# Kernel optimization log

Hardware: AMD Instinct MI355X
Metric: run time of the kernel (lower is better)

Reference implementation:

```python
import jax, jax.numpy as jnp
import numpy as np

B, S, D = 2, 2048, 2048
H, KV, HD = 32, 8, 64
REP = H // KV


def rotate_half(t):
    t1, t2 = t[..., : t.shape[-1] // 2], t[..., t.shape[-1] // 2 :]
    return jnp.concatenate((-t2, t1), axis=-1)


def setup_inputs() -> dict:
    key = jax.random.key(0)
    kx, kq, kk, kv, ko = jax.random.split(key, 5)
    x = jax.random.normal(kx, (B, S, D), dtype=jnp.float32) * 0.02
    # RoPE tables: shape [S, HD//2]; forward concatenates [cos, cos] to reach HD
    inv_freq = 1.0 / (10000.0 ** (np.arange(0, HD, 2, dtype=np.float32) / HD))
    freqs = np.outer(np.arange(S, dtype=np.float32), inv_freq)
    cos = jnp.asarray(np.cos(freqs), dtype=jnp.float32)
    sin = jnp.asarray(np.sin(freqs), dtype=jnp.float32)
    # causal additive mask [1,1,S,S]
    causal = np.tril(np.ones((S, S), dtype=bool))
    mask = jnp.asarray(np.where(causal, 0.0, -1e9).astype(np.float32))[None, None]
    s = 0.02
    wq = jax.random.normal(kq, (H * HD, D), dtype=jnp.float32) * s
    wk = jax.random.normal(kk, (KV * HD, D), dtype=jnp.float32) * s
    wv = jax.random.normal(kv, (KV * HD, D), dtype=jnp.float32) * s
    wo = jax.random.normal(ko, (D, H * HD), dtype=jnp.float32) * s
    return {"x": x, "cos": cos, "sin": sin, "mask": mask,
            "wq": wq, "wk": wk, "wv": wv, "wo": wo}


def reference(x, cos, sin, mask, wq, wk, wv, wo):
    b, s, d = x.shape
    # QKV projections (Linear with bias=False: x @ W^T)
    q = jnp.einsum("bsd,ed->bse", x, wq).reshape(b, s, H, HD)
    k = jnp.einsum("bsd,ed->bse", x, wk).reshape(b, s, KV, HD)
    v = jnp.einsum("bsd,ed->bse", x, wv).reshape(b, s, KV, HD)
    # RoPE: cos/sin [S, HD//2] -> [1, S, 1, HD]
    cc = jnp.concatenate([cos[:s], cos[:s]], axis=-1)[None, :, None, :]
    ss = jnp.concatenate([sin[:s], sin[:s]], axis=-1)[None, :, None, :]
    q = q * cc + rotate_half(q) * ss
    k = k * cc + rotate_half(k) * ss
    # GQA: group q heads by kv head (implicit broadcast instead of repeat_kv)
    q = q.transpose(0, 2, 1, 3).reshape(b, KV, REP, s, HD)  # [B,KV,REP,S,HD]
    k = k.transpose(0, 2, 1, 3)                              # [B,KV,S,HD]
    v = v.transpose(0, 2, 1, 3)                              # [B,KV,S,HD]
    scores = jnp.einsum("bkrqd,bksd->bkrqs", q, k) / np.sqrt(HD)
    scores = scores + mask[:, :, None, :, :]  # broadcast over rep dim
    probs = jax.nn.softmax(scores.astype(jnp.float32), axis=-1).astype(q.dtype)
    out = jnp.einsum("bkrqs,bksd->bkrqd", probs, v)
    out = out.transpose(0, 3, 1, 2, 4).reshape(b, s, H * HD)  # [B,S,H*HD]
    return jnp.einsum("bse,de->bsd", out, wo)
```

## Files before the change

### kernel.cpp

```cpp
#include <hip/hip_runtime.h>
#include <stdint.h>

#define DEV __device__ __forceinline__

typedef __bf16 bf16;
typedef __bf16 bf16x8 __attribute__((ext_vector_type(8)));
typedef __bf16 bf16x4v __attribute__((ext_vector_type(4)));
typedef float f32x4 __attribute__((ext_vector_type(4)));
typedef float f32x16 __attribute__((ext_vector_type(16)));
typedef int int2v __attribute__((ext_vector_type(2)));

constexpr int Bb = 2, Ss = 2048, Dd = 2048, Hh = 32, KVh = 8, HDd = 64;
constexpr int Mm = Bb * Ss;
constexpr int EQ = Hh * HDd;
constexpr int EKV = KVh * HDd;
constexpr int Ee = EQ + 2 * EKV;

DEV void gload16(const void* g, void* l) {
  __builtin_amdgcn_global_load_lds((const __attribute__((address_space(1))) uint32_t*)g,
                                   (__attribute__((address_space(3))) uint32_t*)l, 16, 0, 0);
}

#if __has_builtin(__builtin_amdgcn_exp2f)
DEV float exp2_fast(float x) { return __builtin_amdgcn_exp2f(x); }
#else
DEV float exp2_fast(float x) {
  float r;
  asm("v_exp_f32 %0, %1\n\ts_nop 0" : "=v"(r) : "v"(x));
  return r;
}
#endif
DEV uint32_t cvtpk(float lo, float hi) {
  uint32_t w;
  asm("v_cvt_pk_bf16_f32 %0, %1, %2" : "=v"(w) : "v"(lo), "v"(hi));
  return w;
}
DEV int2v pswap(uint32_t a, uint32_t b) {
  return __builtin_amdgcn_permlane32_swap((int)a, (int)b, false, false);
}
DEV float fu(uint32_t u) { union { uint32_t u; float f; } c; c.u = u; return c.f; }
DEV uint32_t uf(float f) { union { float f; uint32_t u; } c; c.f = f; return c.u; }

__global__ void cvt_kernel(const float* __restrict__ x, const float* __restrict__ wq,
                           const float* __restrict__ wk, const float* __restrict__ wv,
                           const float* __restrict__ wo,
                           bf16* __restrict__ xb, bf16* __restrict__ wqkvb,
                           bf16* __restrict__ wob) {
  const long NX = (long)Mm * Dd;
  const long NQ = (long)EQ * Dd;
  const long NK = (long)EKV * Dd;
  const long NO = (long)Dd * EQ;
  const long total4 = (NX + NQ + 2 * NK + NO) / 4;
  for (long i = (long)blockIdx.x * blockDim.x + threadIdx.x; i < total4;
       i += (long)gridDim.x * blockDim.x) {
    long e = i * 4;
    const float* src; bf16* dst;
    if (e < NX)                { src = x + e;                       dst = xb + e; }
    else if (e < NX + NQ)      { long o = e - NX;                   src = wq + o; dst = wqkvb + o; }
    else if (e < NX + NQ + NK) { long o = e - NX - NQ;              src = wk + o; dst = wqkvb + NQ + o; }
    else if (e < NX + NQ + 2*NK){ long o = e - NX - NQ - NK;        src = wv + o; dst = wqkvb + NQ + NK + o; }
    else                       { long o = e - NX - NQ - 2*NK;       src = wo + o; dst = wob + o; }
    float4 v = *(const float4*)src;
    bf16x4v b;
    b.x = (bf16)v.x; b.y = (bf16)v.y; b.z = (bf16)v.z; b.w = (bf16)v.w;
    *(bf16x4v*)dst = b;
  }
}

__global__ __launch_bounds__(512, 4)
void gemm1_kernel(const bf16* __restrict__ A, const bf16* __restrict__ Bt,
                  bf16* __restrict__ Cb, int Mn, int Nn, int Kn) {
  __shared__ __align__(16) bf16 As[2][128 * 64];
  __shared__ __align__(16) bf16 Bs[2][192 * 64];
  const int tid = threadIdx.x, wid = tid >> 6, lane = tid & 63;
  const int g = lane >> 4, c = lane & 15;
  const int wm = wid >> 2, wn = wid & 3;

  const int xcd = (int)blockIdx.x & 7;
  const int idx = (int)blockIdx.x >> 3;
  const int bi = (xcd >> 1) * 8 + (idx >> 3);
  const int bj = (xcd & 1) * 8 + (idx & 7);
  const long arow0 = (long)bi * 128, brow0 = (long)bj * 192;

  const int srow = tid >> 3, schk = tid & 7;
  const int cs = schk ^ (srow & 7);

  f32x4 acc[4][3] = {};

#pragma unroll
  for (int q = 0; q < 2; ++q)
    gload16(A + (arow0 + q * 64 + srow) * Kn + cs * 8,
            (char*)&As[0][0] + q * 8192 + tid * 16);
#pragma unroll
  for (int q = 0; q < 3; ++q)
    gload16(Bt + (brow0 + q * 64 + srow) * Kn + cs * 8,
            (char*)&Bs[0][0] + q * 8192 + tid * 16);
  __syncthreads();

  const int NT = Kn >> 6;
  for (int kt = 0; kt < NT; ++kt) {
    const char* pa = (const char*)&As[kt & 1][0];
    const char* pb = (const char*)&Bs[kt & 1][0];
    char* na = (char*)&As[(kt + 1) & 1][0];
    char* nb = (char*)&Bs[(kt + 1) & 1][0];
    const bool more = (kt + 1 < NT);

    bf16x8 af[4][2];
#pragma unroll
    for (int i2 = 0; i2 < 4; ++i2)
#pragma unroll
      for (int ks = 0; ks < 2; ++ks) {
        int r = wm * 64 + i2 * 16 + c;
        af[i2][ks] = *(const bf16x8*)(pa + r * 128 + (((ks * 4 + g) ^ (r & 7)) << 4));
      }
    bf16x8 bfr[2];
#pragma unroll
    for (int ks = 0; ks < 2; ++ks) {
      int r = 0 * 64 + wn * 16 + c;
      bfr[ks] = *(const bf16x8*)(pb + r * 128 + (((ks * 4 + g) ^ (r & 7)) << 4));
    }
    if (more) {
      gload16(A + (arow0 + 0 * 64 + srow) * Kn + (kt + 1) * 64 + cs * 8,
              na + 0 * 8192 + tid * 16);
      gload16(A + (arow0 + 1 * 64 + srow) * Kn + (kt + 1) * 64 + cs * 8,
              na + 1 * 8192 + tid * 16);
      gload16(Bt + (brow0 + 0 * 64 + srow) * Kn + (kt + 1) * 64 + cs * 8,
              nb + 0 * 8192 + tid * 16);
    }
    asm volatile("s_waitcnt lgkmcnt(0)" ::: "memory");
    __builtin_amdgcn_s_setprio(1);
#pragma unroll
    for (int i2 = 0; i2 < 4; ++i2)
#pragma unroll
      for (int ks = 0; ks < 2; ++ks)
        acc[i2][0] = __builtin_amdgcn_mfma_f32_16x16x32_bf16(af[i2][ks], bfr[ks],
                                                             acc[i2][0], 0, 0, 0);
    __builtin_amdgcn_s_setprio(0);
    if (more) asm volatile("s_waitcnt vmcnt(4)" ::: "memory");
    else      asm volatile("s_waitcnt vmcnt(1)" ::: "memory");
    __builtin_amdgcn_s_barrier();

#pragma unroll
    for (int ks = 0; ks < 2; ++ks) {
      int r = 1 * 64 + wn * 16 + c;
      bfr[ks] = *(const bf16x8*)(pb + r * 128 + (((ks * 4 + g) ^ (r & 7)) << 4));
    }
    if (more)
      gload16(Bt + (brow0 + 1 * 64 + srow) * Kn + (kt + 1) * 64 + cs * 8,
              nb + 1 * 8192 + tid * 16);
    asm volatile("s_waitcnt lgkmcnt(0)" ::: "memory");
    __builtin_amdgcn_s_setprio(1);
#pragma unroll
    for (int i2 = 0; i2 < 4; ++i2)
#pragma unroll
      for (int ks = 0; ks < 2; ++ks)
        acc[i2][1] = __builtin_amdgcn_mfma_f32_16x16x32_bf16(af[i2][ks], bfr[ks],
                                                             acc[i2][1], 0, 0, 0);
    __builtin_amdgcn_s_setprio(0);
    if (more) asm volatile("s_waitcnt vmcnt(4)" ::: "memory");
    else      asm volatile("s_waitcnt vmcnt(0)" ::: "memory");
    __builtin_amdgcn_s_barrier();

#pragma unroll
    for (int ks = 0; ks < 2; ++ks) {
      int r = 2 * 64 + wn * 16 + c;
      bfr[ks] = *(const bf16x8*)(pb + r * 128 + (((ks * 4 + g) ^ (r & 7)) << 4));
    }
    if (more)
      gload16(Bt + (brow0 + 2 * 64 + srow) * Kn + (kt + 1) * 64 + cs * 8,
              nb + 2 * 8192 + tid * 16);
    asm volatile("s_waitcnt lgkmcnt(0)" ::: "memory");
    __builtin_amdgcn_s_setprio(1);
#pragma unroll
    for (int i2 = 0; i2 < 4; ++i2)
#pragma unroll
      for (int ks = 0; ks < 2; ++ks)
        acc[i2][2] = __builtin_amdgcn_mfma_f32_16x16x32_bf16(af[i2][ks], bfr[ks],
                                                             acc[i2][2], 0, 0, 0);
    __builtin_amdgcn_s_setprio(0);
    if (more) {
      asm volatile("s_waitcnt vmcnt(2)" ::: "memory");
      __builtin_amdgcn_s_barrier();
    }
  }

#pragma unroll
  for (int i = 0; i < 4; ++i)
#pragma unroll
    for (int j = 0; j < 3; ++j)
#pragma unroll
      for (int r = 0; r < 4; ++r) {
        long row = arow0 + wm * 64 + i * 16 + 4 * g + r;
        long col = brow0 + j * 64 + wn * 16 + c;
        Cb[row * Nn + col] = (bf16)acc[i][j][r];
      }
}

__global__ __launch_bounds__(512, 4)
void gemm2_kernel(const bf16* __restrict__ A, const bf16* __restrict__ Bt,
                  float* __restrict__ Cf, int Mn, int Nn, int Kn) {
  __shared__ __align__(16) bf16 As[2][128 * 64];
  __shared__ __align__(16) bf16 Bs[2][128 * 64];
  const int tid = threadIdx.x, wid = tid >> 6, lane = tid & 63;
  const int g = lane >> 4, c = lane & 15;
  const int wm = wid >> 2, wn = wid & 3;

  const int xcd = (int)blockIdx.x & 7;
  const int idx = (int)blockIdx.x >> 3;
  const int bi = (xcd >> 1) * 8 + (idx >> 3);
  const int bj = (xcd & 1) * 8 + (idx & 7);
  const long arow0 = (long)bi * 128, brow0 = (long)bj * 128;

  const int srow = tid >> 3, schk = tid & 7;
  const int cs = schk ^ (srow & 7);

  f32x4 acc[4][2] = {};

#pragma unroll
  for (int q = 0; q < 2; ++q) {
    gload16(A + (arow0 + q * 64 + srow) * Kn + cs * 8,
            (char*)&As[0][0] + q * 8192 + tid * 16);
    gload16(Bt + (brow0 + q * 64 + srow) * Kn + cs * 8,
            (char*)&Bs[0][0] + q * 8192 + tid * 16);
  }
  __syncthreads();

  const int NT = Kn >> 6;
  for (int kt = 0; kt < NT; ++kt) {
    const char* pa = (const char*)&As[kt & 1][0];
    const char* pb = (const char*)&Bs[kt & 1][0];
    char* na = (char*)&As[(kt + 1) & 1][0];
    char* nb = (char*)&Bs[(kt + 1) & 1][0];
    const bool more = (kt + 1 < NT);

    bf16x8 af[4][2];
#pragma unroll
    for (int i2 = 0; i2 < 4; ++i2)
#pragma unroll
      for (int ks = 0; ks < 2; ++ks) {
        int r = wm * 64 + i2 * 16 + c;
        af[i2][ks] = *(const bf16x8*)(pa + r * 128 + (((ks * 4 + g) ^ (r & 7)) << 4));
      }
    bf16x8 bfr[2];
#pragma unroll
    for (int ks = 0; ks < 2; ++ks) {
      int r = 0 * 64 + wn * 16 + c;
      bfr[ks] = *(const bf16x8*)(pb + r * 128 + (((ks * 4 + g) ^ (r & 7)) << 4));
    }
    if (more) {
      gload16(A + (arow0 + 0 * 64 + srow) * Kn + (kt + 1) * 64 + cs * 8,
              na + 0 * 8192 + tid * 16);
      gload16(Bt + (brow0 + 0 * 64 + srow) * Kn + (kt + 1) * 64 + cs * 8,
              nb + 0 * 8192 + tid * 16);
    }
    asm volatile("s_waitcnt lgkmcnt(0)" ::: "memory");
    __builtin_amdgcn_s_setprio(1);
#pragma unroll
    for (int i2 = 0; i2 < 4; ++i2)
#pragma unroll
      for (int ks = 0; ks < 2; ++ks)
        acc[i2][0] = __builtin_amdgcn_mfma_f32_16x16x32_bf16(af[i2][ks], bfr[ks],
                                                             acc[i2][0], 0, 0, 0);
    __builtin_amdgcn_s_setprio(0);
    if (more) asm volatile("s_waitcnt vmcnt(2)" ::: "memory");
    else      asm volatile("s_waitcnt vmcnt(0)" ::: "memory");
    __builtin_amdgcn_s_barrier();

#pragma unroll
    for (int ks = 0; ks < 2; ++ks) {
      int r = 1 * 64 + wn * 16 + c;
      bfr[ks] = *(const bf16x8*)(pb + r * 128 + (((ks * 4 + g) ^ (r & 7)) << 4));
    }
    if (more) {
      gload16(A + (arow0 + 1 * 64 + srow) * Kn + (kt + 1) * 64 + cs * 8,
              na + 1 * 8192 + tid * 16);
      gload16(Bt + (brow0 + 1 * 64 + srow) * Kn + (kt + 1) * 64 + cs * 8,
              nb + 1 * 8192 + tid * 16);
    }
    asm volatile("s_waitcnt lgkmcnt(0)" ::: "memory");
    __builtin_amdgcn_s_setprio(1);
#pragma unroll
    for (int i2 = 0; i2 < 4; ++i2)
#pragma unroll
      for (int ks = 0; ks < 2; ++ks)
        acc[i2][1] = __builtin_amdgcn_mfma_f32_16x16x32_bf16(af[i2][ks], bfr[ks],
                                                             acc[i2][1], 0, 0, 0);
    __builtin_amdgcn_s_setprio(0);
    if (more) {
      asm volatile("s_waitcnt vmcnt(1)" ::: "memory");
      __builtin_amdgcn_s_barrier();
    }
  }

#pragma unroll
  for (int i = 0; i < 4; ++i)
#pragma unroll
    for (int j = 0; j < 2; ++j)
#pragma unroll
      for (int r = 0; r < 4; ++r) {
        long row = arow0 + wm * 64 + i * 16 + 4 * g + r;
        long col = brow0 + j * 64 + wn * 16 + c;
        Cf[row * Nn + col] = acc[i][j][r];
      }
}

__global__ void kv_prep_kernel(const bf16* __restrict__ qkv, const float* __restrict__ cosT,
                               const float* __restrict__ sinT, bf16* __restrict__ kout,
                               bf16* __restrict__ vtb) {
  if (blockIdx.x < 512) {
    __shared__ __align__(16) unsigned short tile[64][72];
    int blk = blockIdx.x;
    int st = blk & 31, kvh = (blk >> 5) & 7, b = blk >> 8;
    int s0 = st * 64;
    int t = threadIdx.x;
#pragma unroll
    for (int rep = 0; rep < 2; ++rep) {
      int idx = t + rep * 256;
      int r = idx >> 3, cb = idx & 7;
      const bf16* src = qkv + ((long)(b * Ss + s0 + r)) * Ee + EQ + EKV + kvh * 64 + cb * 8;
      *(uint4*)&tile[r][cb * 8] = *(const uint4*)src;
    }
    __syncthreads();
#pragma unroll
    for (int rep = 0; rep < 2; ++rep) {
      int idx = t + rep * 256;
      int dd = idx >> 3, scb = idx & 7;
      union { unsigned short u[8]; uint4 v; } pk;
#pragma unroll
      for (int j = 0; j < 8; ++j) pk.u[j] = tile[scb * 8 + j][dd];
      long dst = ((long)((b * KVh + kvh) * 64 + dd)) * Ss + s0 + scb * 8;
      *(uint4*)&vtb[dst] = pk.v;
    }
  } else {
    int tid = (int)(blockIdx.x - 512) * blockDim.x + threadIdx.x;
    int d = tid & 31;
    int h = (tid >> 5) & (KVh - 1);
    int m = tid >> 8;
    if (m >= Mm) return;
    int s = m & (Ss - 1), b = m >> 11;
    float lo = (float)qkv[(long)m * Ee + EQ + h * 64 + d];
    float hi = (float)qkv[(long)m * Ee + EQ + h * 64 + d + 32];
    float cs = cosT[s * 32 + d], sn = sinT[s * 32 + d];
    long base = (((long)(b * KVh + h)) * Ss + s) * 64;
    kout[base + d]      = (bf16)(lo * cs - hi * sn);
    kout[base + d + 32] = (bf16)(hi * cs + lo * sn);
  }
}

__global__ __launch_bounds__(512)
void attn_kernel(const bf16* __restrict__ qkv, const float* __restrict__ cosT,
                 const float* __restrict__ sinT, const bf16* __restrict__ k,
                 const bf16* __restrict__ vt, bf16* __restrict__ o) {
  __shared__ __align__(16) bf16 Kt[2][2][64 * 64];
  __shared__ __align__(16) bf16 Vt[2][2][64 * 64];
  constexpr float SCL = 0.18033688f;

  const int tid = threadIdx.x, qw = tid >> 6, lane = tid & 63;
  const int ql = lane & 31, hi = lane >> 5;
  const int g6 = (int)(blockIdx.x >> 6);
  const int qt = (g6 < 4) ? (7 - g6) : (g6 - 4);
  const int bh = blockIdx.x & 63;
  const int b = bh >> 5, h = bh & 31;
  const int kvh = h >> 2;
  const int q0 = qt * 256;
  const int qw_q0 = q0 + qw * 32;

  const bf16* kbase = k + ((long)(b * KVh + kvh)) * Ss * 64;
  const bf16* vbase = vt + ((long)(b * KVh + kvh)) * 64 * Ss;

  const int srow = tid >> 3, scb = tid & 7;
  const int scbs = scb ^ (srow & 7);
  const int sdst = tid * 16;

  bf16x8 qf[4];
  {
    const int s_row = q0 + qw * 32 + ql;
    const bf16* qrow = qkv + ((long)(b * Ss + s_row)) * Ee + h * 64 + 8 * hi;
    bf16x8 qraw[4];
#pragma unroll
    for (int ks = 0; ks < 4; ++ks) qraw[ks] = *(const bf16x8*)(qrow + 16 * ks);
    float cs8[2][8], sn8[2][8];
#pragma unroll
    for (int ks2 = 0; ks2 < 2; ++ks2) {
      const float* cp = cosT + s_row * 32 + 16 * ks2 + 8 * hi;
      const float* sp = sinT + s_row * 32 + 16 * ks2 + 8 * hi;
      *(float4*)&cs8[ks2][0] = *(const float4*)cp;
      *(float4*)&cs8[ks2][4] = *(const float4*)(cp + 4);
      *(float4*)&sn8[ks2][0] = *(const float4*)sp;
      *(float4*)&sn8[ks2][4] = *(const float4*)(sp + 4);
    }
#pragma unroll
    for (int ks2 = 0; ks2 < 2; ++ks2)
#pragma unroll
      for (int j = 0; j < 8; ++j) {
        float lo = (float)qraw[ks2][j], hv = (float)qraw[ks2 + 2][j];
        qf[ks2][j]     = (bf16)((lo * cs8[ks2][j] - hv * sn8[ks2][j]) * SCL);
        qf[ks2 + 2][j] = (bf16)((hv * cs8[ks2][j] + lo * sn8[ks2][j]) * SCL);
      }
  }

  bf16x8 bones;
#pragma unroll
  for (int j = 0; j < 8; ++j) bones[j] = (bf16)1.0f;

  gload16(kbase + (long)srow * 64 + scbs * 8, (char*)&Kt[0][0][0] + sdst);
  gload16(kbase + ((long)64 + srow) * 64 + scbs * 8, (char*)&Kt[0][1][0] + sdst);
  gload16(vbase + (long)srow * Ss + scbs * 8, (char*)&Vt[0][0][0] + sdst);
  gload16(vbase + (long)srow * Ss + 64 + scbs * 8, (char*)&Vt[0][1][0] + sdst);
  __syncthreads();

  f32x16 Oacc0 = {}, Oacc1 = {}, lacc = {};
  const int qa = qw_q0 + ql;
  const int nt = 4 * qt + 4;
  const int ntp = nt >> 1;
  const int tdiag = qw_q0 >> 6;

  int cur = 0;
  for (int pp = 0; pp < ntp; ++pp) {
    if (pp + 1 < ntp) {
      int nb = cur ^ 1;
      long t0 = (long)(2 * pp + 2) * 64;
      gload16(kbase + (t0 + srow) * 64 + scbs * 8, (char*)&Kt[nb][0][0] + sdst);
      gload16(kbase + (t0 + 64 + srow) * 64 + scbs * 8, (char*)&Kt[nb][1][0] + sdst);
      gload16(vbase + (long)srow * Ss + t0 + scbs * 8, (char*)&Vt[nb][0][0] + sdst);
      gload16(vbase + (long)srow * Ss + t0 + 64 + scbs * 8, (char*)&Vt[nb][1][0] + sdst);
    }

#pragma unroll
    for (int half = 0; half < 2; ++half) {
      const int t = 2 * pp + half;
      if (64 * t < qw_q0 + 32) {
        f32x16 s0 = {}, s1 = {};
        const char* kt = (const char*)&Kt[cur][half][0];
#pragma unroll
        for (int ks = 0; ks < 4; ++ks) {
          int chk = ((2 * ks + hi) ^ (ql & 7)) << 4;
          bf16x8 kf0 = *(const bf16x8*)(kt + ql * 128 + chk);
          bf16x8 kf1 = *(const bf16x8*)(kt + (32 + ql) * 128 + chk);
          s0 = __builtin_amdgcn_mfma_f32_32x32x16_bf16(kf0, qf[ks], s0, 0, 0, 0);
          s1 = __builtin_amdgcn_mfma_f32_32x32x16_bf16(kf1, qf[ks], s1, 0, 0, 0);
        }

        if (t == tdiag) {
#pragma unroll
          for (int r = 0; r < 16; ++r) {
            int kv0 = t * 64 + (r & 3) + 8 * (r >> 2) + 4 * hi;
            if (kv0 > qa)      s0[r] = -1e30f;
            if (kv0 + 32 > qa) s1[r] = -1e30f;
          }
        }

#pragma unroll
        for (int r = 0; r < 16; ++r) {
          s0[r] = exp2_fast(s0[r]);
          s1[r] = exp2_fast(s1[r]);
        }

        const char* vtb0 = (const char*)&Vt[cur][half][0];
#pragma unroll
        for (int ks = 0; ks < 4; ++ks) {
          uint32_t pk01, pk23, pk45, pk67;
          if (ks < 2) {
            const int rb = (ks & 1) * 8;
            pk01 = cvtpk(s0[rb + 0], s0[rb + 1]);
            pk23 = cvtpk(s0[rb + 2], s0[rb + 3]);
            pk45 = cvtpk(s0[rb + 4], s0[rb + 5]);
            pk67 = cvtpk(s0[rb + 6], s0[rb + 7]);
          } else {
            const int rb = (ks & 1) * 8;
            pk01 = cvtpk(s1[rb + 0], s1[rb + 1]);
            pk23 = cvtpk(s1[rb + 2], s1[rb + 3]);
            pk45 = cvtpk(s1[rb + 4], s1[rb + 5]);
            pk67 = cvtpk(s1[rb + 6], s1[rb + 7]);
          }
          int2v w02 = pswap(pk01, pk45);
          int2v w13 = pswap(pk23, pk67);
          union { uint32_t u[4]; bf16x8 v; } pa;
          pa.u[0] = (uint32_t)w02.x; pa.u[1] = (uint32_t)w13.x;
          pa.u[2] = (uint32_t)w02.y; pa.u[3] = (uint32_t)w13.y;

          int chk = ((2 * ks + hi) ^ (ql & 7)) << 4;
          bf16x8 vf0 = *(const bf16x8*)(vtb0 + ql * 128 + chk);
          bf16x8 vf1 = *(const bf16x8*)(vtb0 + (32 + ql) * 128 + chk);
          Oacc0 = __builtin_amdgcn_mfma_f32_32x32x16_bf16(pa.v, vf0, Oacc0, 0, 0, 0);
          Oacc1 = __builtin_amdgcn_mfma_f32_32x32x16_bf16(pa.v, vf1, Oacc1, 0, 0, 0);
          lacc  = __builtin_amdgcn_mfma_f32_32x32x16_bf16(pa.v, bones, lacc, 0, 0, 0);
        }
      }
    }

    __syncthreads();
    cur ^= 1;
  }

#pragma unroll
  for (int r = 0; r < 16; ++r) {
    int qrow = (r & 3) + 8 * (r >> 2) + 4 * hi;
    float li = 1.0f / lacc[r];
    long orow = (long)b * Ss + q0 + 32 * qw + qrow;
    o[orow * EQ + h * 64 + ql]      = (bf16)(Oacc0[r] * li);
    o[orow * EQ + h * 64 + 32 + ql] = (bf16)(Oacc1[r] * li);
  }
}

extern "C" void kernel_launch(void* const* d_in, const int* in_sizes, int n_in,
                              void* d_out, int out_size, void* d_ws, size_t ws_size,
                              hipStream_t stream) {
  const float* x    = (const float*)d_in[0];
  const float* cosT = (const float*)d_in[1];
  const float* sinT = (const float*)d_in[2];
  const float* wq   = (const float*)d_in[4];
  const float* wk   = (const float*)d_in[5];
  const float* wv   = (const float*)d_in[6];
  const float* wo   = (const float*)d_in[7];

  if (ws_size < 104857600u) return;

  char* ws = (char*)d_ws;
  bf16* xb    = (bf16*)(ws + 0);
  bf16* wqkvb = (bf16*)(ws + 16777216);
  bf16* wob   = (bf16*)(ws + 29360128);
  bf16* qkvb  = (bf16*)(ws + 37748736);
  bf16* kb    = (bf16*)(ws + 79691776);
  bf16* vtb   = (bf16*)(ws + 83886080);
  bf16* attnb = (bf16*)(ws + 88080384);
  float* outp = (float*)d_out;

  cvt_kernel<<<dim3(2048), dim3(256), 0, stream>>>(x, wq, wk, wv, wo, xb, wqkvb, wob);
  gemm1_kernel<<<dim3((Mm / 128) * (Ee / 192)), dim3(512), 0, stream>>>(
      xb, wqkvb, qkvb, Mm, Ee, Dd);
  kv_prep_kernel<<<dim3(512 + (Mm * KVh * 32) / 256), dim3(256), 0, stream>>>(
      qkvb, cosT, sinT, kb, vtb);
  attn_kernel<<<dim3(512), dim3(512), 0, stream>>>(qkvb, cosT, sinT, kb, vtb, attnb);
  gemm2_kernel<<<dim3((Mm / 128) * (EQ / 128)), dim3(512), 0, stream>>>(
      attnb, wob, outp, Mm, EQ, EQ);
}
```

Measured before the change: 158.6 us.

## Triple-buffer K tiles and prefetch two steps ahead with partial vmcnt waits

Adds a third LDS buffer for K so K tiles are prefetched two iterations ahead while V stays double-buffered. The full __syncthreads is replaced by an s_waitcnt vmcnt(2)/vmcnt(0) plus a raw s_barrier, so the loads for the furthest K tile can stay in flight across the barrier. This aims to hide global-to-LDS load latency behind the MFMA work. It raises LDS use, which may lower occupancy, and relies on the counts of outstanding loads being right.

```diff
diff --git a/kernel.cpp b/kernel.cpp
--- a/kernel.cpp
+++ b/kernel.cpp
@@ -351,7 +351,7 @@
 void attn_kernel(const bf16* __restrict__ qkv, const float* __restrict__ cosT,
                  const float* __restrict__ sinT, const bf16* __restrict__ k,
                  const bf16* __restrict__ vt, bf16* __restrict__ o) {
-  __shared__ __align__(16) bf16 Kt[2][2][64 * 64];
+  __shared__ __align__(16) bf16 Kt[3][2][64 * 64];
   __shared__ __align__(16) bf16 Vt[2][2][64 * 64];
   constexpr float SCL = 0.18033688f;
 
@@ -403,27 +403,38 @@
 #pragma unroll
   for (int j = 0; j < 8; ++j) bones[j] = (bf16)1.0f;
 
-  gload16(kbase + (long)srow * 64 + scbs * 8, (char*)&Kt[0][0][0] + sdst);
-  gload16(kbase + ((long)64 + srow) * 64 + scbs * 8, (char*)&Kt[0][1][0] + sdst);
-  gload16(vbase + (long)srow * Ss + scbs * 8, (char*)&Vt[0][0][0] + sdst);
-  gload16(vbase + (long)srow * Ss + 64 + scbs * 8, (char*)&Vt[0][1][0] + sdst);
-  __syncthreads();
-
   f32x16 Oacc0 = {}, Oacc1 = {}, lacc = {};
   const int qa = qw_q0 + ql;
   const int nt = 4 * qt + 4;
   const int ntp = nt >> 1;
   const int tdiag = qw_q0 >> 6;
 
-  int cur = 0;
+  gload16(kbase + (long)srow * 64 + scbs * 8, (char*)&Kt[0][0][0] + sdst);
+  gload16(kbase + ((long)64 + srow) * 64 + scbs * 8, (char*)&Kt[0][1][0] + sdst);
+  if (1 < ntp) {
+    gload16(kbase + ((long)128 + srow) * 64 + scbs * 8, (char*)&Kt[1][0][0] + sdst);
+    gload16(kbase + ((long)192 + srow) * 64 + scbs * 8, (char*)&Kt[1][1][0] + sdst);
+  }
+  gload16(vbase + (long)srow * Ss + scbs * 8, (char*)&Vt[0][0][0] + sdst);
+  gload16(vbase + (long)srow * Ss + 64 + scbs * 8, (char*)&Vt[0][1][0] + sdst);
+  __syncthreads();
+
+  int kc = 0;
   for (int pp = 0; pp < ntp; ++pp) {
-    if (pp + 1 < ntp) {
-      int nb = cur ^ 1;
-      long t0 = (long)(2 * pp + 2) * 64;
-      gload16(kbase + (t0 + srow) * 64 + scbs * 8, (char*)&Kt[nb][0][0] + sdst);
-      gload16(kbase + (t0 + 64 + srow) * 64 + scbs * 8, (char*)&Kt[nb][1][0] + sdst);
-      gload16(vbase + (long)srow * Ss + t0 + scbs * 8, (char*)&Vt[nb][0][0] + sdst);
-      gload16(vbase + (long)srow * Ss + t0 + 64 + scbs * 8, (char*)&Vt[nb][1][0] + sdst);
+    const int vc = pp & 1;
+    const bool moreV = (pp + 1 < ntp);
+    const bool moreK = (pp + 2 < ntp);
+
+    if (moreV) {
+      long t0 = (long)(pp + 1) * 128;
+      gload16(vbase + (long)srow * Ss + t0 + scbs * 8, (char*)&Vt[vc ^ 1][0][0] + sdst);
+      gload16(vbase + (long)srow * Ss + t0 + 64 + scbs * 8, (char*)&Vt[vc ^ 1][1][0] + sdst);
+    }
+    if (moreK) {
+      int ks3 = kc + 2; if (ks3 >= 3) ks3 -= 3;
+      long t0 = (long)(pp + 2) * 128;
+      gload16(kbase + (t0 + srow) * 64 + scbs * 8, (char*)&Kt[ks3][0][0] + sdst);
+      gload16(kbase + (t0 + 64 + srow) * 64 + scbs * 8, (char*)&Kt[ks3][1][0] + sdst);
     }
 
 #pragma unroll
@@ -431,7 +442,7 @@
       const int t = 2 * pp + half;
       if (64 * t < qw_q0 + 32) {
         f32x16 s0 = {}, s1 = {};
-        const char* kt = (const char*)&Kt[cur][half][0];
+        const char* kt = (const char*)&Kt[kc][half][0];
 #pragma unroll
         for (int ks = 0; ks < 4; ++ks) {
           int chk = ((2 * ks + hi) ^ (ql & 7)) << 4;
@@ -456,7 +467,7 @@
           s1[r] = exp2_fast(s1[r]);
         }
 
-        const char* vtb0 = (const char*)&Vt[cur][half][0];
+        const char* vtb0 = (const char*)&Vt[vc][half][0];
 #pragma unroll
         for (int ks = 0; ks < 4; ++ks) {
           uint32_t pk01, pk23, pk45, pk67;
@@ -489,8 +500,10 @@
       }
     }
 
-    __syncthreads();
-    cur ^= 1;
+    if (moreK) asm volatile("s_waitcnt vmcnt(2)" ::: "memory");
+    else       asm volatile("s_waitcnt vmcnt(0)" ::: "memory");
+    __builtin_amdgcn_s_barrier();
+    kc = (kc + 1 == 3) ? 0 : kc + 1;
   }
 
 #pragma unroll
```

Measured after the change: 157.4 us (median of 3 runs). Within noise of the previous version (-0.8%).
